# Kernel optimization log

Hardware: AMD Instinct MI355X
Metric: run time of the kernel (lower is better)

## Reference

```python
import jax, jax.numpy as jnp
import numpy as np

B, S, H, NH = 2, 2048, 1024, 16
HD = H // NH
ROTARY_DIM = 64
EPS = 1e-5
MINUS_INF = -10000.0


def _apply_rotary(q, k, rotary_dim):
    # q, k: [B, S, NH, HD]; GPT-NeoX style rotate_half on first rotary_dim dims
    pos = jnp.arange(S, dtype=jnp.float32)
    inv_freq = 1.0 / (10000.0 ** (jnp.arange(0, rotary_dim, 2, dtype=jnp.float32) / rotary_dim))
    freqs = pos[:, None] * inv_freq[None, :]                      # [S, rd/2]
    cos = jnp.concatenate([jnp.cos(freqs)] * 2, -1)[None, :, None, :]  # [1,S,1,rd]
    sin = jnp.concatenate([jnp.sin(freqs)] * 2, -1)[None, :, None, :]

    def rot(t):
        t_rot, t_pass = t[..., :rotary_dim], t[..., rotary_dim:]
        t1, t2 = jnp.split(t_rot, 2, axis=-1)
        rotated = jnp.concatenate([-t2, t1], axis=-1)
        return jnp.concatenate([t_rot * cos + rotated * sin, t_pass], axis=-1)

    return rot(q), rot(k)


def setup_inputs() -> dict:
    key = jax.random.key(0)
    ks = jax.random.split(key, 6)
    w_scale = 0.02
    return {
        "x": jax.random.normal(ks[0], (B, S, H), jnp.float32),
        "input_mask": jnp.ones((B, S), jnp.int32),
        "norm_w": jnp.ones((H,), jnp.float32),
        "norm_b": jnp.zeros((H,), jnp.float32),
        "attn_qkvw": jax.random.normal(ks[1], (H, 3 * H), jnp.float32) * w_scale,
        "attn_qkvb": jax.random.normal(ks[2], (3 * H,), jnp.float32) * w_scale,
        "attn_ow": jax.random.normal(ks[3], (H, H), jnp.float32) * w_scale,
        "attn_ob": jax.random.normal(ks[4], (H,), jnp.float32) * w_scale,
    }


def reference(x, input_mask, norm_w, norm_b, attn_qkvw, attn_qkvb, attn_ow, attn_ob):
    # pre-layernorm (qkv_gemm path with config.pre_layer_norm)
    mu = x.mean(-1, keepdims=True)
    var = x.var(-1, keepdims=True)
    xn = (x - mu) * jax.lax.rsqrt(var + EPS) * norm_w + norm_b

    # fused QKV projection
    qkv = xn @ attn_qkvw + attn_qkvb                       # [B,S,3H]
    q, k, v = jnp.split(qkv, 3, axis=-1)
    q = q.reshape(B, S, NH, HD)
    k = k.reshape(B, S, NH, HD)
    v = v.reshape(B, S, NH, HD)

    # rotary embedding on q,k
    q, k = _apply_rotary(q, k, ROTARY_DIM)

    # scaled scores + mask bias (1 - mask) * -10000 + triangular masking
    scale = 1.0 / np.sqrt(HD).astype(np.float32)
    scores = jnp.einsum("bqhd,bkhd->bhqk", q, k) * scale   # [B,NH,S,S]
    mask_bias = (1.0 - input_mask.astype(scores.dtype)) * MINUS_INF
    scores = scores + mask_bias[:, None, None, :]
    causal = jnp.tril(jnp.ones((S, S), bool))
    scores = jnp.where(causal[None, None], scores, MINUS_INF)

    probs = jax.nn.softmax(scores, axis=-1)
    ctx = jnp.einsum("bhqk,bkhd->bqhd", probs, v).reshape(B, S, H)

    # output projection (vector_matmul + bias)
    return ctx @ attn_ow + attn_ob
```

## Files before the change

kernel.cpp:

```cpp
#include <hip/hip_runtime.h>
#include <hip/hip_bf16.h>

#define B_  2
#define S_  2048
#define H_  1024
#define NH_ 16
#define HD_ 64
#define T_  (B_*S_)
#define H3_ (3*H_)

typedef float  floatx4 __attribute__((ext_vector_type(4)));
typedef __bf16 bf16x8  __attribute__((ext_vector_type(8)));

__device__ inline unsigned short f2bf_rn(float f) {
    union { float f; unsigned int u; } v; v.f = f;
    unsigned int u = v.u;
    u += 0x7fffu + ((u >> 16) & 1u);
    return (unsigned short)(u >> 16);
}
__device__ inline unsigned short f2bf_tr(float f) {
    union { float f; unsigned int u; } v; v.f = f;
    return (unsigned short)(v.u >> 16);
}
__device__ inline floatx4 fzero4() { floatx4 v; v[0]=0.f; v[1]=0.f; v[2]=0.f; v[3]=0.f; return v; }

__device__ inline void gload_lds16(const unsigned short* g, unsigned short* l) {
    __builtin_amdgcn_global_load_lds((const __attribute__((address_space(1))) unsigned int*)g,
                                     (__attribute__((address_space(3))) unsigned int*)l,
                                     16, 0, 0);
}

#define TLD 72
__global__ __launch_bounds__(256) void cvt_both_k(const float* __restrict__ qkvw,
                                                  const float* __restrict__ ow,
                                                  unsigned short* __restrict__ qkvwT,
                                                  unsigned short* __restrict__ owT) {
    __shared__ unsigned short Ts[64 * TLD];
    int id = blockIdx.x;
    const float* W; unsigned short* Wt; int N, nb, kb;
    if (id < 768) { W = qkvw; Wt = qkvwT; N = H3_; nb = (id % 48) * 64; kb = (id / 48) * 64; }
    else { id -= 768; W = ow; Wt = owT; N = H_; nb = (id % 16) * 64; kb = (id / 16) * 64; }
    const int K = H_;
    const int tid = threadIdx.x;
    #pragma unroll
    for (int p = 0; p < 4; p++) {
        const int krow = kb + p * 16 + (tid >> 4);
        const int ncol = (tid & 15) * 4;
        const float4 w = *reinterpret_cast<const float4*>(&W[(size_t)krow * N + nb + ncol]);
        Ts[(ncol + 0) * TLD + p * 16 + (tid >> 4)] = f2bf_rn(w.x);
        Ts[(ncol + 1) * TLD + p * 16 + (tid >> 4)] = f2bf_rn(w.y);
        Ts[(ncol + 2) * TLD + p * 16 + (tid >> 4)] = f2bf_rn(w.z);
        Ts[(ncol + 3) * TLD + p * 16 + (tid >> 4)] = f2bf_rn(w.w);
    }
    __syncthreads();
    #pragma unroll
    for (int p = 0; p < 2; p++) {
        const int n = (tid >> 3) + p * 32;
        const int k8 = (tid & 7) * 8;
        const uint4 v = *reinterpret_cast<const uint4*>(&Ts[n * TLD + k8]);
        *reinterpret_cast<uint4*>(&Wt[(size_t)(nb + n) * K + kb + k8]) = v;
    }
}

__global__ __launch_bounds__(256) void layernorm_k(const float* __restrict__ x,
                                                   const float* __restrict__ w,
                                                   const float* __restrict__ b,
                                                   unsigned short* __restrict__ xn) {
    const int t   = blockIdx.x;
    const int tid = threadIdx.x;
    const float4 v = reinterpret_cast<const float4*>(x + (size_t)t * H_)[tid];
    float s  = v.x + v.y + v.z + v.w;
    float s2 = v.x*v.x + v.y*v.y + v.z*v.z + v.w*v.w;
    for (int off = 32; off > 0; off >>= 1) {
        s  += __shfl_down(s,  off, 64);
        s2 += __shfl_down(s2, off, 64);
    }
    __shared__ float red[8];
    const int wave = tid >> 6, lane = tid & 63;
    if (lane == 0) { red[wave] = s; red[4 + wave] = s2; }
    __syncthreads();
    if (tid == 0) {
        red[0] = red[0] + red[1] + red[2] + red[3];
        red[4] = red[4] + red[5] + red[6] + red[7];
    }
    __syncthreads();
    const float mean = red[0] * (1.f / H_);
    const float var  = red[4] * (1.f / H_) - mean * mean;
    const float rstd = rsqrtf(var + 1e-5f);
    const float4 wv = reinterpret_cast<const float4*>(w)[tid];
    const float4 bv = reinterpret_cast<const float4*>(b)[tid];
    ushort4 o = make_ushort4(f2bf_rn((v.x - mean) * rstd * wv.x + bv.x),
                             f2bf_rn((v.y - mean) * rstd * wv.y + bv.y),
                             f2bf_rn((v.z - mean) * rstd * wv.z + bv.z),
                             f2bf_rn((v.w - mean) * rstd * wv.w + bv.w));
    reinterpret_cast<ushort4*>(xn + (size_t)t * H_)[tid] = o;
}

#define BM 128
#define BN 128

__device__ inline void gemm_core(const unsigned short* __restrict__ A,
                                 const unsigned short* __restrict__ Bt,
                                 int K, int mBase, int nBase,
                                 int tid, floatx4 acc[4][4],
                                 unsigned short* As0, unsigned short* As1,
                                 unsigned short* Bs0, unsigned short* Bs1) {
    const int lane = tid & 63;
    const int wave = tid >> 6;
    const int wr = wave >> 1, wc = wave & 1;
    const int srow = lane >> 2;
    const int scol = (lane & 3) * 8;
    const int mrow = lane & 15;
    const int koff = (lane >> 4) * 8;

    for (int kb = 0; kb < K; kb += 64) {
        __syncthreads();
        #pragma unroll
        for (int p = 0; p < 2; p++) {
            const int r = wave * 16 + p * 64;
            const size_t ga = (size_t)(mBase + r + srow) * K + kb + scol;
            const size_t gb = (size_t)(nBase + r + srow) * K + kb + scol;
            gload_lds16(&A [ga],      &As0[r * 32]);
            gload_lds16(&A [ga + 32], &As1[r * 32]);
            gload_lds16(&Bt[gb],      &Bs0[r * 32]);
            gload_lds16(&Bt[gb + 32], &Bs1[r * 32]);
        }
        __syncthreads();

        #pragma unroll
        for (int half = 0; half < 2; half++) {
            const unsigned short* As = half ? As1 : As0;
            const unsigned short* Bs = half ? Bs1 : Bs0;
            bf16x8 afrag[4], bfrag[4];
            #pragma unroll
            for (int mt = 0; mt < 4; mt++)
                afrag[mt] = *reinterpret_cast<const bf16x8*>(&As[(wr * 64 + mt * 16 + mrow) * 32 + koff]);
            #pragma unroll
            for (int nt = 0; nt < 4; nt++)
                bfrag[nt] = *reinterpret_cast<const bf16x8*>(&Bs[(wc * 64 + nt * 16 + mrow) * 32 + koff]);
            #pragma unroll
            for (int mt = 0; mt < 4; mt++)
                #pragma unroll
                for (int nt = 0; nt < 4; nt++)
                    acc[mt][nt] = __builtin_amdgcn_mfma_f32_16x16x32_bf16(afrag[mt], bfrag[nt], acc[mt][nt], 0, 0, 0);
        }
    }
}

__global__ __launch_bounds__(256) void gemm_qkv_k(const unsigned short* __restrict__ A,
                                                  const unsigned short* __restrict__ Bt,
                                                  const float* __restrict__ bias,
                                                  unsigned short* __restrict__ Qo,
                                                  unsigned short* __restrict__ Ko,
                                                  unsigned short* __restrict__ Vto) {
    __shared__ unsigned short As0[BM * 32], As1[BM * 32];
    __shared__ unsigned short Bs0[BN * 32], Bs1[BN * 32];

    const int tid  = threadIdx.x;
    const int lane = tid & 63;
    const int wave = tid >> 6;
    const int wr = wave >> 1, wc = wave & 1;
    const int mBase = blockIdx.y * BM;
    const int nBase = blockIdx.x * BN;

    floatx4 acc[4][4];
    #pragma unroll
    for (int i = 0; i < 4; i++)
        #pragma unroll
        for (int j = 0; j < 4; j++) acc[i][j] = fzero4();

    gemm_core(A, Bt, H_, mBase, nBase, tid, acc, As0, As1, Bs0, Bs1);

    const int col0 = lane & 15;
    const int r0   = (lane >> 4) * 4;
    const int hg   = (nBase + wc * 64) >> 6;
    const int sec  = hg >> 4;
    const int h    = hg & 15;

    float bs[4];
    #pragma unroll
    for (int nt = 0; nt < 4; nt++) bs[nt] = bias[nBase + wc * 64 + nt * 16 + col0];

    if (sec < 2) {
        unsigned short* dst = (sec == 0) ? Qo : Ko;
        const float if0 = __expf((float)col0        * (-0.2878231366f));
        const float if1 = __expf((float)(16 + col0) * (-0.2878231366f));
        #pragma unroll
        for (int mt = 0; mt < 4; mt++) {
            #pragma unroll
            for (int reg = 0; reg < 4; reg++) {
                const int t  = mBase + wr * 64 + mt * 16 + r0 + reg;
                const int bb = t >> 11;
                const int s  = t & (S_ - 1);
                float sn0, cs0, sn1, cs1;
                __sincosf((float)s * if0, &sn0, &cs0);
                __sincosf((float)s * if1, &sn1, &cs1);
                const float v0 = acc[mt][0][reg] + bs[0];
                const float v1 = acc[mt][1][reg] + bs[1];
                const float v2 = acc[mt][2][reg] + bs[2];
                const float v3 = acc[mt][3][reg] + bs[3];
                const float o0 = v0 * cs0 - v2 * sn0;
                const float o1 = v1 * cs1 - v3 * sn1;
                const float o2 = v2 * cs0 + v0 * sn0;
                const float o3 = v3 * cs1 + v1 * sn1;
                const size_t rb = ((size_t)(bb * NH_ + h) * S_ + s) * HD_;
                dst[rb +      col0] = f2bf_rn(o0);
                dst[rb + 16 + col0] = f2bf_rn(o1);
                dst[rb + 32 + col0] = f2bf_rn(o2);
                dst[rb + 48 + col0] = f2bf_rn(o3);
            }
        }
    } else {
        #pragma unroll
        for (int mt = 0; mt < 4; mt++) {
            const int t0 = mBase + wr * 64 + mt * 16 + r0;
            const int bb = t0 >> 11;
            const int s0 = t0 & (S_ - 1);
            #pragma unroll
            for (int nt = 0; nt < 4; nt++) {
                const int d = nt * 16 + col0;
                ushort4 o;
                o.x = f2bf_rn(acc[mt][nt][0] + bs[nt]);
                o.y = f2bf_rn(acc[mt][nt][1] + bs[nt]);
                o.z = f2bf_rn(acc[mt][nt][2] + bs[nt]);
                o.w = f2bf_rn(acc[mt][nt][3] + bs[nt]);
                *reinterpret_cast<ushort4*>(&Vto[((size_t)(bb * NH_ + h) * HD_ + d) * S_ + s0]) = o;
            }
        }
    }
}

__global__ __launch_bounds__(256) void gemm_proj_k(const unsigned short* __restrict__ A,
                                                   const unsigned short* __restrict__ Bt,
                                                   const float* __restrict__ bias,
                                                   float* __restrict__ Cf,
                                                   int M, int N, int K) {
    __shared__ unsigned short As0[BM * 32], As1[BM * 32];
    __shared__ unsigned short Bs0[BN * 32], Bs1[BN * 32];

    const int tid  = threadIdx.x;
    const int lane = tid & 63;
    const int wave = tid >> 6;
    const int wr = wave >> 1, wc = wave & 1;
    const int mBase = blockIdx.y * BM;
    const int nBase = blockIdx.x * BN;

    floatx4 acc[4][4];
    #pragma unroll
    for (int i = 0; i < 4; i++)
        #pragma unroll
        for (int j = 0; j < 4; j++) acc[i][j] = fzero4();

    gemm_core(A, Bt, K, mBase, nBase, tid, acc, As0, As1, Bs0, Bs1);

    const int col0 = lane & 15;
    const int r0   = (lane >> 4) * 4;
    #pragma unroll
    for (int mt = 0; mt < 4; mt++) {
        #pragma unroll
        for (int nt = 0; nt < 4; nt++) {
            const int gcol = nBase + wc * 64 + nt * 16 + col0;
            const float bsv = bias[gcol];
            #pragma unroll
            for (int reg = 0; reg < 4; reg++) {
                const int grow = mBase + wr * 64 + mt * 16 + r0 + reg;
                Cf[(size_t)grow * N + gcol] = acc[mt][nt][reg] + bsv;
            }
        }
    }
}

#define ALD 72
#define SCL2 0.1803368801f
#define MNEG -14427.0f

__global__ __launch_bounds__(256, 3) void attn_k(const unsigned short* __restrict__ Q,
                                                 const unsigned short* __restrict__ Kg,
                                                 const unsigned short* __restrict__ Vt,
                                                 const int* __restrict__ mask,
                                                 unsigned short* __restrict__ ctx) {
    const int id = blockIdx.x;
    const int bh = id & 31;
    const int v  = 31 - (id >> 5);
    const int b  = bh >> 4;
    const int h  = bh & 15;
    const int tid  = threadIdx.x;
    const int lane = tid & 63;
    const int wave = tid >> 6;

    __shared__ unsigned short Ks [2][64 * ALD];
    __shared__ unsigned short Vts[2][64 * ALD];
    __shared__ unsigned short Ps[4][16 * ALD];

    const size_t base = (size_t)bh * S_ * HD_;
    const int qbase = v * 64 + wave * 16;
    const int mrow = lane & 15;
    const int koff = (lane >> 4) * 8;
    const int r0   = (lane >> 4) * 4;
    const int col0 = lane & 15;

    bf16x8 qf0 = *reinterpret_cast<const bf16x8*>(&Q[base + (size_t)(qbase + mrow) * HD_ + koff]);
    bf16x8 qf1 = *reinterpret_cast<const bf16x8*>(&Q[base + (size_t)(qbase + mrow) * HD_ + 32 + koff]);

    bf16x8 onesf;
    {
        const __bf16 ov = (__bf16)((mrow == 0) ? 1.f : 0.f);
        #pragma unroll
        for (int q = 0; q < 8; q++) onesf[q] = ov;
    }

    floatx4 Oacc[4];
    floatx4 Lacc = fzero4();
    #pragma unroll
    for (int nt = 0; nt < 4; nt++) Oacc[nt] = fzero4();

    const int srow = tid >> 3;
    const int scol = (tid & 7) * 8;

    uint4 k00, k01, k10, k11, v00, v01, v10, v11;
    float mb00, mb01, mb02, mb03, mb10, mb11, mb12, mb13;
#define PF_TILE(TT, KR0, KR1, VR0, VR1, M0, M1, M2, M3) do {                                   \
        const int kb_ = (TT) * 64;                                                             \
        KR0 = *reinterpret_cast<const uint4*>(&Kg[base + (size_t)(kb_ + srow)      * HD_ + scol]); \
        KR1 = *reinterpret_cast<const uint4*>(&Kg[base + (size_t)(kb_ + srow + 32) * HD_ + scol]); \
        VR0 = *reinterpret_cast<const uint4*>(&Vt[base + (size_t)srow        * S_ + kb_ + scol]);  \
        VR1 = *reinterpret_cast<const uint4*>(&Vt[base + (size_t)(srow + 32) * S_ + kb_ + scol]);  \
        M0 = (1.f - (float)mask[b * S_ + kb_ +  0 + col0]) * MNEG;                             \
        M1 = (1.f - (float)mask[b * S_ + kb_ + 16 + col0]) * MNEG;                             \
        M2 = (1.f - (float)mask[b * S_ + kb_ + 32 + col0]) * MNEG;                             \
        M3 = (1.f - (float)mask[b * S_ + kb_ + 48 + col0]) * MNEG;                             \
    } while (0)
#define PREFETCH_MACRO(MI) do {                                                                \
        const int t0_ = min(2 * (MI), v);                                                      \
        const int t1_ = min(2 * (MI) + 1, v);                                                  \
        PF_TILE(t0_, k00, k01, v00, v01, mb00, mb01, mb02, mb03);                              \
        PF_TILE(t1_, k10, k11, v10, v11, mb10, mb11, mb12, mb13);                              \
    } while (0)

    const int nmac = (v + 2) >> 1;
    PREFETCH_MACRO(0);

    unsigned short* pw = Ps[wave];

    for (int mi = 0; mi < nmac; mi++) {
        if (mi) __syncthreads();
        *reinterpret_cast<uint4*>(&Ks [0][ srow       * ALD + scol]) = k00;
        *reinterpret_cast<uint4*>(&Ks [0][(srow + 32) * ALD + scol]) = k01;
        *reinterpret_cast<uint4*>(&Ks [1][ srow       * ALD + scol]) = k10;
        *reinterpret_cast<uint4*>(&Ks [1][(srow + 32) * ALD + scol]) = k11;
        *reinterpret_cast<uint4*>(&Vts[0][ srow       * ALD + scol]) = v00;
        *reinterpret_cast<uint4*>(&Vts[0][(srow + 32) * ALD + scol]) = v01;
        *reinterpret_cast<uint4*>(&Vts[1][ srow       * ALD + scol]) = v10;
        *reinterpret_cast<uint4*>(&Vts[1][(srow + 32) * ALD + scol]) = v11;
        __syncthreads();
        const float mc00 = mb00, mc01 = mb01, mc02 = mb02, mc03 = mb03;
        const float mc10 = mb10, mc11 = mb11, mc12 = mb12, mc13 = mb13;
        if (mi + 1 < nmac) PREFETCH_MACRO(mi + 1);

        #pragma unroll
        for (int half = 0; half < 2; half++) {
            const int kt = 2 * mi + half;
            if (half && kt > v) continue;
            const int kb = kt * 64;
            const unsigned short* ks = Ks [half];
            const unsigned short* vs = Vts[half];
            const float c0 = half ? mc10 : mc00;
            const float c1 = half ? mc11 : mc01;
            const float c2 = half ? mc12 : mc02;
            const float c3 = half ? mc13 : mc03;

            floatx4 sc[4];
            #pragma unroll
            for (int nt = 0; nt < 4; nt++) {
                const bf16x8 kf0 = *reinterpret_cast<const bf16x8*>(&ks[(nt * 16 + mrow) * ALD + koff]);
                const bf16x8 kf1 = *reinterpret_cast<const bf16x8*>(&ks[(nt * 16 + mrow) * ALD + 32 + koff]);
                floatx4 c = fzero4();
                c = __builtin_amdgcn_mfma_f32_16x16x32_bf16(qf0, kf0, c, 0, 0, 0);
                c = __builtin_amdgcn_mfma_f32_16x16x32_bf16(qf1, kf1, c, 0, 0, 0);
                sc[nt] = c;
            }
            #pragma unroll
            for (int nt = 0; nt < 4; nt++) {
                const float mbv = (nt == 0) ? c0 : (nt == 1) ? c1 : (nt == 2) ? c2 : c3;
                #pragma unroll
                for (int reg = 0; reg < 4; reg++)
                    sc[nt][reg] = sc[nt][reg] * SCL2 + mbv;
            }
            if (kt == v) {
                #pragma unroll
                for (int nt = 0; nt < 4; nt++) {
                    const int key = kb + nt * 16 + col0;
                    #pragma unroll
                    for (int reg = 0; reg < 4; reg++)
                        if (key > qbase + r0 + reg) sc[nt][reg] = MNEG;
                }
            }
            #pragma unroll
            for (int nt = 0; nt < 4; nt++)
                #pragma unroll
                for (int reg = 0; reg < 4; reg++)
                    pw[(r0 + reg) * ALD + nt * 16 + col0] = f2bf_tr(exp2f(sc[nt][reg]));
            const bf16x8 p0 = *reinterpret_cast<const bf16x8*>(&pw[mrow * ALD + koff]);
            const bf16x8 p1 = *reinterpret_cast<const bf16x8*>(&pw[mrow * ALD + 32 + koff]);
            #pragma unroll
            for (int nt = 0; nt < 4; nt++) {
                const bf16x8 vf0 = *reinterpret_cast<const bf16x8*>(&vs[(nt * 16 + mrow) * ALD + koff]);
                const bf16x8 vf1 = *reinterpret_cast<const bf16x8*>(&vs[(nt * 16 + mrow) * ALD + 32 + koff]);
                Oacc[nt] = __builtin_amdgcn_mfma_f32_16x16x32_bf16(p0, vf0, Oacc[nt], 0, 0, 0);
                Oacc[nt] = __builtin_amdgcn_mfma_f32_16x16x32_bf16(p1, vf1, Oacc[nt], 0, 0, 0);
            }
            Lacc = __builtin_amdgcn_mfma_f32_16x16x32_bf16(p0, onesf, Lacc, 0, 0, 0);
            Lacc = __builtin_amdgcn_mfma_f32_16x16x32_bf16(p1, onesf, Lacc, 0, 0, 0);
        }
    }
#undef PREFETCH_MACRO
#undef PF_TILE

    float rl[4];
    #pragma unroll
    for (int reg = 0; reg < 4; reg++) {
        const float lsum = __shfl(Lacc[reg], lane & 48, 64);
        rl[reg] = 1.f / lsum;
    }
    #pragma unroll
    for (int nt = 0; nt < 4; nt++)
        #pragma unroll
        for (int reg = 0; reg < 4; reg++) {
            const int q = qbase + r0 + reg;
            const int d = nt * 16 + col0;
            ctx[((size_t)b * S_ + q) * H_ + h * HD_ + d] = f2bf_rn(Oacc[nt][reg] * rl[reg]);
        }
}

extern "C" void kernel_launch(void* const* d_in, const int* in_sizes, int n_in,
                              void* d_out, int out_size, void* d_ws, size_t ws_size,
                              hipStream_t stream) {
    const float* x     = (const float*)d_in[0];
    const int*   mask  = (const int*)d_in[1];
    const float* normw = (const float*)d_in[2];
    const float* normb = (const float*)d_in[3];
    const float* qkvw  = (const float*)d_in[4];
    const float* qkvb  = (const float*)d_in[5];
    const float* ow    = (const float*)d_in[6];
    const float* ob    = (const float*)d_in[7];
    float* out = (float*)d_out;

    char* ws = (char*)d_ws;
    unsigned short* xn_bf   = (unsigned short*)(ws);
    unsigned short* qkvwT   = (unsigned short*)(ws + (8ull  << 20));
    unsigned short* owT     = (unsigned short*)(ws + (14ull << 20));
    unsigned short* Qb      = (unsigned short*)(ws + (16ull << 20));
    unsigned short* Kb      = (unsigned short*)(ws + (24ull << 20));
    unsigned short* Vtb     = (unsigned short*)(ws + (32ull << 20));
    unsigned short* ctx_bf  = (unsigned short*)(ws + (40ull << 20));

    cvt_both_k<<<1024, 256, 0, stream>>>(qkvw, ow, qkvwT, owT);
    layernorm_k<<<T_, 256, 0, stream>>>(x, normw, normb, xn_bf);
    gemm_qkv_k<<<dim3(H3_ / BN, T_ / BM), 256, 0, stream>>>(xn_bf, qkvwT, qkvb, Qb, Kb, Vtb);
    attn_k<<<1024, 256, 0, stream>>>(Qb, Kb, Vtb, mask, ctx_bf);
    gemm_proj_k<<<dim3(H_ / BN, T_ / BM), 256, 0, stream>>>(ctx_bf, owT, ob, out, T_, H_, H_);
}
```

Before: 200.6 us.

## Double attention query tile per block to 128 rows and reorder causal blocks

Each wave now processes 32 query rows (two 16-row MFMA groups) instead of 16, so a block covers 128 queries. Each K/V tile loaded into shared memory is therefore reused for twice as many score and PV MFMAs, cutting global loads and LDS staging per query. The grid is halved to 512 blocks, and the block order is remapped so the first 256 blocks go from heavy to light work and the rest from light to heavy, to balance the causal workload. In exchange it doubles accumulator registers and lowers the occupancy hint from 3 to 2 blocks, and the coarser tiles raise the tail imbalance.

```diff
diff --git a/kernel.cpp b/kernel.cpp
--- a/kernel.cpp
+++ b/kernel.cpp
@@ -274,14 +274,15 @@
 #define SCL2 0.1803368801f
 #define MNEG -14427.0f
 
-__global__ __launch_bounds__(256, 3) void attn_k(const unsigned short* __restrict__ Q,
+__global__ __launch_bounds__(256, 2) void attn_k(const unsigned short* __restrict__ Q,
                                                  const unsigned short* __restrict__ Kg,
                                                  const unsigned short* __restrict__ Vt,
                                                  const int* __restrict__ mask,
                                                  unsigned short* __restrict__ ctx) {
     const int id = blockIdx.x;
-    const int bh = id & 31;
-    const int v  = 31 - (id >> 5);
+    int bh, v;
+    if (id < 256) { bh = id & 31; v = 15 - (id >> 5); }
+    else { const int i2 = id - 256; bh = i2 & 31; v = i2 >> 5; }
     const int b  = bh >> 4;
     const int h  = bh & 15;
     const int tid  = threadIdx.x;
@@ -290,17 +291,21 @@
 
     __shared__ unsigned short Ks [2][64 * ALD];
     __shared__ unsigned short Vts[2][64 * ALD];
-    __shared__ unsigned short Ps[4][16 * ALD];
+    __shared__ unsigned short Ps [4][32 * ALD];
 
     const size_t base = (size_t)bh * S_ * HD_;
-    const int qbase = v * 64 + wave * 16;
+    const int qbase = v * 128 + wave * 32;
     const int mrow = lane & 15;
     const int koff = (lane >> 4) * 8;
     const int r0   = (lane >> 4) * 4;
     const int col0 = lane & 15;
 
-    bf16x8 qf0 = *reinterpret_cast<const bf16x8*>(&Q[base + (size_t)(qbase + mrow) * HD_ + koff]);
-    bf16x8 qf1 = *reinterpret_cast<const bf16x8*>(&Q[base + (size_t)(qbase + mrow) * HD_ + 32 + koff]);
+    bf16x8 qf[2][2];
+    #pragma unroll
+    for (int mg = 0; mg < 2; mg++) {
+        qf[mg][0] = *reinterpret_cast<const bf16x8*>(&Q[base + (size_t)(qbase + mg * 16 + mrow) * HD_ + koff]);
+        qf[mg][1] = *reinterpret_cast<const bf16x8*>(&Q[base + (size_t)(qbase + mg * 16 + mrow) * HD_ + 32 + koff]);
+    }
 
     bf16x8 onesf;
     {
@@ -309,13 +314,20 @@
         for (int q = 0; q < 8; q++) onesf[q] = ov;
     }
 
-    floatx4 Oacc[4];
-    floatx4 Lacc = fzero4();
-    #pragma unroll
-    for (int nt = 0; nt < 4; nt++) Oacc[nt] = fzero4();
+    floatx4 Oacc[2][4];
+    floatx4 Lacc[2];
+    #pragma unroll
+    for (int mg = 0; mg < 2; mg++) {
+        Lacc[mg] = fzero4();
+        #pragma unroll
+        for (int nt = 0; nt < 4; nt++) Oacc[mg][nt] = fzero4();
+    }
 
     const int srow = tid >> 3;
     const int scol = (tid & 7) * 8;
+
+    const int vmaxt = 2 * v + 1;
+    const int vlast = 2 * v + (wave >> 1);
 
     uint4 k00, k01, k10, k11, v00, v01, v10, v11;
     float mb00, mb01, mb02, mb03, mb10, mb11, mb12, mb13;
@@ -331,13 +343,13 @@
         M3 = (1.f - (float)mask[b * S_ + kb_ + 48 + col0]) * MNEG;                             \
     } while (0)
 #define PREFETCH_MACRO(MI) do {                                                                \
-        const int t0_ = min(2 * (MI), v);                                                      \
-        const int t1_ = min(2 * (MI) + 1, v);                                                  \
+        const int t0_ = min(2 * (MI), vmaxt);                                                  \
+        const int t1_ = min(2 * (MI) + 1, vmaxt);                                              \
         PF_TILE(t0_, k00, k01, v00, v01, mb00, mb01, mb02, mb03);                              \
         PF_TILE(t1_, k10, k11, v10, v11, mb10, mb11, mb12, mb13);                              \
     } while (0)
 
-    const int nmac = (v + 2) >> 1;
+    const int nmac = v + 1;
     PREFETCH_MACRO(0);
 
     unsigned short* pw = Ps[wave];
@@ -360,7 +372,7 @@
         #pragma unroll
         for (int half = 0; half < 2; half++) {
             const int kt = 2 * mi + half;
-            if (half && kt > v) continue;
+            if (half && kt > vlast) continue;
             const int kb = kt * 64;
             const unsigned short* ks = Ks [half];
             const unsigned short* vs = Vts[half];
@@ -369,67 +381,89 @@
             const float c2 = half ? mc12 : mc02;
             const float c3 = half ? mc13 : mc03;
 
-            floatx4 sc[4];
+            floatx4 sc[2][4];
             #pragma unroll
             for (int nt = 0; nt < 4; nt++) {
                 const bf16x8 kf0 = *reinterpret_cast<const bf16x8*>(&ks[(nt * 16 + mrow) * ALD + koff]);
                 const bf16x8 kf1 = *reinterpret_cast<const bf16x8*>(&ks[(nt * 16 + mrow) * ALD + 32 + koff]);
-                floatx4 c = fzero4();
-                c = __builtin_amdgcn_mfma_f32_16x16x32_bf16(qf0, kf0, c, 0, 0, 0);
-                c = __builtin_amdgcn_mfma_f32_16x16x32_bf16(qf1, kf1, c, 0, 0, 0);
-                sc[nt] = c;
-            }
-            #pragma unroll
-            for (int nt = 0; nt < 4; nt++) {
-                const float mbv = (nt == 0) ? c0 : (nt == 1) ? c1 : (nt == 2) ? c2 : c3;
-                #pragma unroll
-                for (int reg = 0; reg < 4; reg++)
-                    sc[nt][reg] = sc[nt][reg] * SCL2 + mbv;
-            }
-            if (kt == v) {
+                #pragma unroll
+                for (int mg = 0; mg < 2; mg++) {
+                    floatx4 c = fzero4();
+                    c = __builtin_amdgcn_mfma_f32_16x16x32_bf16(qf[mg][0], kf0, c, 0, 0, 0);
+                    c = __builtin_amdgcn_mfma_f32_16x16x32_bf16(qf[mg][1], kf1, c, 0, 0, 0);
+                    sc[mg][nt] = c;
+                }
+            }
+            #pragma unroll
+            for (int mg = 0; mg < 2; mg++)
                 #pragma unroll
                 for (int nt = 0; nt < 4; nt++) {
-                    const int key = kb + nt * 16 + col0;
+                    const float mbv = (nt == 0) ? c0 : (nt == 1) ? c1 : (nt == 2) ? c2 : c3;
                     #pragma unroll
                     for (int reg = 0; reg < 4; reg++)
-                        if (key > qbase + r0 + reg) sc[nt][reg] = MNEG;
+                        sc[mg][nt][reg] = sc[mg][nt][reg] * SCL2 + mbv;
                 }
-            }
-            #pragma unroll
-            for (int nt = 0; nt < 4; nt++)
-                #pragma unroll
-                for (int reg = 0; reg < 4; reg++)
-                    pw[(r0 + reg) * ALD + nt * 16 + col0] = f2bf_tr(exp2f(sc[nt][reg]));
-            const bf16x8 p0 = *reinterpret_cast<const bf16x8*>(&pw[mrow * ALD + koff]);
-            const bf16x8 p1 = *reinterpret_cast<const bf16x8*>(&pw[mrow * ALD + 32 + koff]);
+            if (kt == vlast) {
+                #pragma unroll
+                for (int mg = 0; mg < 2; mg++)
+                    #pragma unroll
+                    for (int nt = 0; nt < 4; nt++) {
+                        const int key = kb + nt * 16 + col0;
+                        #pragma unroll
+                        for (int reg = 0; reg < 4; reg++)
+                            if (key > qbase + mg * 16 + r0 + reg) sc[mg][nt][reg] = MNEG;
+                    }
+            }
+            #pragma unroll
+            for (int mg = 0; mg < 2; mg++)
+                #pragma unroll
+                for (int nt = 0; nt < 4; nt++)
+                    #pragma unroll
+                    for (int reg = 0; reg < 4; reg++)
+                        pw[(mg * 16 + r0 + reg) * ALD + nt * 16 + col0] = f2bf_tr(exp2f(sc[mg][nt][reg]));
+            bf16x8 p0[2], p1[2];
+            #pragma unroll
+            for (int mg = 0; mg < 2; mg++) {
+                p0[mg] = *reinterpret_cast<const bf16x8*>(&pw[(mg * 16 + mrow) * ALD + koff]);
+                p1[mg] = *reinterpret_cast<const bf16x8*>(&pw[(mg * 16 + mrow) * ALD + 32 + koff]);
+            }
             #pragma unroll
             for (int nt = 0; nt < 4; nt++) {
                 const bf16x8 vf0 = *reinterpret_cast<const bf16x8*>(&vs[(nt * 16 + mrow) * ALD + koff]);
                 const bf16x8 vf1 = *reinterpret_cast<const bf16x8*>(&vs[(nt * 16 + mrow) * ALD + 32 + koff]);
-                Oacc[nt] = __builtin_amdgcn_mfma_f32_16x16x32_bf16(p0, vf0, Oacc[nt], 0, 0, 0);
-                Oacc[nt] = __builtin_amdgcn_mfma_f32_16x16x32_bf16(p1, vf1, Oacc[nt], 0, 0, 0);
-            }
-            Lacc = __builtin_amdgcn_mfma_f32_16x16x32_bf16(p0, onesf, Lacc, 0, 0, 0);
-            Lacc = __builtin_amdgcn_mfma_f32_16x16x32_bf16(p1, onesf, Lacc, 0, 0, 0);
+                #pragma unroll
+                for (int mg = 0; mg < 2; mg++) {
+                    Oacc[mg][nt] = __builtin_amdgcn_mfma_f32_16x16x32_bf16(p0[mg], vf0, Oacc[mg][nt], 0, 0, 0);
+                    Oacc[mg][nt] = __builtin_amdgcn_mfma_f32_16x16x32_bf16(p1[mg], vf1, Oacc[mg][nt], 0, 0, 0);
+                }
+            }
+            #pragma unroll
+            for (int mg = 0; mg < 2; mg++) {
+                Lacc[mg] = __builtin_amdgcn_mfma_f32_16x16x32_bf16(p0[mg], onesf, Lacc[mg], 0, 0, 0);
+                Lacc[mg] = __builtin_amdgcn_mfma_f32_16x16x32_bf16(p1[mg], onesf, Lacc[mg], 0, 0, 0);
+            }
         }
     }
 #undef PREFETCH_MACRO
 #undef PF_TILE
 
-    float rl[4];
-    #pragma unroll
-    for (int reg = 0; reg < 4; reg++) {
-        const float lsum = __shfl(Lacc[reg], lane & 48, 64);
-        rl[reg] = 1.f / lsum;
-    }
-    #pragma unroll
-    for (int nt = 0; nt < 4; nt++)
+    #pragma unroll
+    for (int mg = 0; mg < 2; mg++) {
+        float rl[4];
         #pragma unroll
         for (int reg = 0; reg < 4; reg++) {
-            const int q = qbase + r0 + reg;
-            const int d = nt * 16 + col0;
-            ctx[((size_t)b * S_ + q) * H_ + h * HD_ + d] = f2bf_rn(Oacc[nt][reg] * rl[reg]);
-        }
+            const float lsum = __shfl(Lacc[mg][reg], lane & 48, 64);
+            rl[reg] = 1.f / lsum;
+        }
+        #pragma unroll
+        for (int nt = 0; nt < 4; nt++)
+            #pragma unroll
+            for (int reg = 0; reg < 4; reg++) {
+                const int q = qbase + mg * 16 + r0 + reg;
+                const int d = nt * 16 + col0;
+                ctx[((size_t)b * S_ + q) * H_ + h * HD_ + d] = f2bf_rn(Oacc[mg][nt][reg] * rl[reg]);
+            }
+    }
 }
 
 extern "C" void kernel_launch(void* const* d_in, const int* in_sizes, int n_in,
@@ -457,6 +491,6 @@
     cvt_both_k<<<1024, 256, 0, stream>>>(qkvw, ow, qkvwT, owT);
     layernorm_k<<<T_, 256, 0, stream>>>(x, normw, normb, xn_bf);
     gemm_qkv_k<<<dim3(H3_ / BN, T_ / BM), 256, 0, stream>>>(xn_bf, qkvwT, qkvb, Qb, Kb, Vtb);
-    attn_k<<<1024, 256, 0, stream>>>(Qb, Kb, Vtb, mask, ctx_bf);
+    attn_k<<<512, 256, 0, stream>>>(Qb, Kb, Vtb, mask, ctx_bf);
     gemm_proj_k<<<dim3(H_ / BN, T_ / BM), 256, 0, stream>>>(ctx_bf, owT, ob, out, T_, H_, H_);
 }
```

Measured after the change: 208.6 us. 1.04x slower.

## Load K and V fragments directly from global memory in attention kernel

Applied to the files above, without the earlier changes.

Removes the shared-memory staging of K and V tiles, the register prefetch pipeline and the block-wide barriers. Each wave now reads its MFMA operand fragments for K and Vt straight from global memory, relying on L1/L2 to serve the reuse across the four waves. Occupancy is also raised from 3 to 4 blocks per CU. In exchange it loses explicit prefetch overlap and issues four times the global/L1 traffic for K and V, since the waves no longer share a staged copy.

```diff
diff --git a/kernel.cpp b/kernel.cpp
--- a/kernel.cpp
+++ b/kernel.cpp
@@ -274,7 +274,7 @@
 #define SCL2 0.1803368801f
 #define MNEG -14427.0f
 
-__global__ __launch_bounds__(256, 3) void attn_k(const unsigned short* __restrict__ Q,
+__global__ __launch_bounds__(256, 4) void attn_k(const unsigned short* __restrict__ Q,
                                                  const unsigned short* __restrict__ Kg,
                                                  const unsigned short* __restrict__ Vt,
                                                  const int* __restrict__ mask,
@@ -288,8 +288,6 @@
     const int lane = tid & 63;
     const int wave = tid >> 6;
 
-    __shared__ unsigned short Ks [2][64 * ALD];
-    __shared__ unsigned short Vts[2][64 * ALD];
     __shared__ unsigned short Ps[4][16 * ALD];
 
     const size_t base = (size_t)bh * S_ * HD_;
@@ -299,8 +297,8 @@
     const int r0   = (lane >> 4) * 4;
     const int col0 = lane & 15;
 
-    bf16x8 qf0 = *reinterpret_cast<const bf16x8*>(&Q[base + (size_t)(qbase + mrow) * HD_ + koff]);
-    bf16x8 qf1 = *reinterpret_cast<const bf16x8*>(&Q[base + (size_t)(qbase + mrow) * HD_ + 32 + koff]);
+    const bf16x8 qf0 = *reinterpret_cast<const bf16x8*>(&Q[base + (size_t)(qbase + mrow) * HD_ + koff]);
+    const bf16x8 qf1 = *reinterpret_cast<const bf16x8*>(&Q[base + (size_t)(qbase + mrow) * HD_ + 32 + koff]);
 
     bf16x8 onesf;
     {
@@ -314,107 +312,59 @@
     #pragma unroll
     for (int nt = 0; nt < 4; nt++) Oacc[nt] = fzero4();
 
-    const int srow = tid >> 3;
-    const int scol = (tid & 7) * 8;
-
-    uint4 k00, k01, k10, k11, v00, v01, v10, v11;
-    float mb00, mb01, mb02, mb03, mb10, mb11, mb12, mb13;
-#define PF_TILE(TT, KR0, KR1, VR0, VR1, M0, M1, M2, M3) do {                                   \
-        const int kb_ = (TT) * 64;                                                             \
-        KR0 = *reinterpret_cast<const uint4*>(&Kg[base + (size_t)(kb_ + srow)      * HD_ + scol]); \
-        KR1 = *reinterpret_cast<const uint4*>(&Kg[base + (size_t)(kb_ + srow + 32) * HD_ + scol]); \
-        VR0 = *reinterpret_cast<const uint4*>(&Vt[base + (size_t)srow        * S_ + kb_ + scol]);  \
-        VR1 = *reinterpret_cast<const uint4*>(&Vt[base + (size_t)(srow + 32) * S_ + kb_ + scol]);  \
-        M0 = (1.f - (float)mask[b * S_ + kb_ +  0 + col0]) * MNEG;                             \
-        M1 = (1.f - (float)mask[b * S_ + kb_ + 16 + col0]) * MNEG;                             \
-        M2 = (1.f - (float)mask[b * S_ + kb_ + 32 + col0]) * MNEG;                             \
-        M3 = (1.f - (float)mask[b * S_ + kb_ + 48 + col0]) * MNEG;                             \
-    } while (0)
-#define PREFETCH_MACRO(MI) do {                                                                \
-        const int t0_ = min(2 * (MI), v);                                                      \
-        const int t1_ = min(2 * (MI) + 1, v);                                                  \
-        PF_TILE(t0_, k00, k01, v00, v01, mb00, mb01, mb02, mb03);                              \
-        PF_TILE(t1_, k10, k11, v10, v11, mb10, mb11, mb12, mb13);                              \
-    } while (0)
-
-    const int nmac = (v + 2) >> 1;
-    PREFETCH_MACRO(0);
-
     unsigned short* pw = Ps[wave];
 
-    for (int mi = 0; mi < nmac; mi++) {
-        if (mi) __syncthreads();
-        *reinterpret_cast<uint4*>(&Ks [0][ srow       * ALD + scol]) = k00;
-        *reinterpret_cast<uint4*>(&Ks [0][(srow + 32) * ALD + scol]) = k01;
-        *reinterpret_cast<uint4*>(&Ks [1][ srow       * ALD + scol]) = k10;
-        *reinterpret_cast<uint4*>(&Ks [1][(srow + 32) * ALD + scol]) = k11;
-        *reinterpret_cast<uint4*>(&Vts[0][ srow       * ALD + scol]) = v00;
-        *reinterpret_cast<uint4*>(&Vts[0][(srow + 32) * ALD + scol]) = v01;
-        *reinterpret_cast<uint4*>(&Vts[1][ srow       * ALD + scol]) = v10;
-        *reinterpret_cast<uint4*>(&Vts[1][(srow + 32) * ALD + scol]) = v11;
-        __syncthreads();
-        const float mc00 = mb00, mc01 = mb01, mc02 = mb02, mc03 = mb03;
-        const float mc10 = mb10, mc11 = mb11, mc12 = mb12, mc13 = mb13;
-        if (mi + 1 < nmac) PREFETCH_MACRO(mi + 1);
-
-        #pragma unroll
-        for (int half = 0; half < 2; half++) {
-            const int kt = 2 * mi + half;
-            if (half && kt > v) continue;
-            const int kb = kt * 64;
-            const unsigned short* ks = Ks [half];
-            const unsigned short* vs = Vts[half];
-            const float c0 = half ? mc10 : mc00;
-            const float c1 = half ? mc11 : mc01;
-            const float c2 = half ? mc12 : mc02;
-            const float c3 = half ? mc13 : mc03;
-
-            floatx4 sc[4];
+    for (int kt = 0; kt <= v; kt++) {
+        const int kb = kt * 64;
+
+        const float c0 = (1.f - (float)mask[b * S_ + kb +  0 + col0]) * MNEG;
+        const float c1 = (1.f - (float)mask[b * S_ + kb + 16 + col0]) * MNEG;
+        const float c2 = (1.f - (float)mask[b * S_ + kb + 32 + col0]) * MNEG;
+        const float c3 = (1.f - (float)mask[b * S_ + kb + 48 + col0]) * MNEG;
+
+        floatx4 sc[4];
+        #pragma unroll
+        for (int nt = 0; nt < 4; nt++) {
+            const bf16x8 kf0 = *reinterpret_cast<const bf16x8*>(&Kg[base + (size_t)(kb + nt * 16 + mrow) * HD_ + koff]);
+            const bf16x8 kf1 = *reinterpret_cast<const bf16x8*>(&Kg[base + (size_t)(kb + nt * 16 + mrow) * HD_ + 32 + koff]);
+            floatx4 c = fzero4();
+            c = __builtin_amdgcn_mfma_f32_16x16x32_bf16(qf0, kf0, c, 0, 0, 0);
+            c = __builtin_amdgcn_mfma_f32_16x16x32_bf16(qf1, kf1, c, 0, 0, 0);
+            sc[nt] = c;
+        }
+        #pragma unroll
+        for (int nt = 0; nt < 4; nt++) {
+            const float mbv = (nt == 0) ? c0 : (nt == 1) ? c1 : (nt == 2) ? c2 : c3;
+            #pragma unroll
+            for (int reg = 0; reg < 4; reg++)
+                sc[nt][reg] = sc[nt][reg] * SCL2 + mbv;
+        }
+        if (kt == v) {
             #pragma unroll
             for (int nt = 0; nt < 4; nt++) {
-                const bf16x8 kf0 = *reinterpret_cast<const bf16x8*>(&ks[(nt * 16 + mrow) * ALD + koff]);
-                const bf16x8 kf1 = *reinterpret_cast<const bf16x8*>(&ks[(nt * 16 + mrow) * ALD + 32 + koff]);
-                floatx4 c = fzero4();
-                c = __builtin_amdgcn_mfma_f32_16x16x32_bf16(qf0, kf0, c, 0, 0, 0);
-                c = __builtin_amdgcn_mfma_f32_16x16x32_bf16(qf1, kf1, c, 0, 0, 0);
-                sc[nt] = c;
-            }
-            #pragma unroll
-            for (int nt = 0; nt < 4; nt++) {
-                const float mbv = (nt == 0) ? c0 : (nt == 1) ? c1 : (nt == 2) ? c2 : c3;
+                const int key = kb + nt * 16 + col0;
                 #pragma unroll
                 for (int reg = 0; reg < 4; reg++)
-                    sc[nt][reg] = sc[nt][reg] * SCL2 + mbv;
+                    if (key > qbase + r0 + reg) sc[nt][reg] = MNEG;
             }
-            if (kt == v) {
-                #pragma unroll
-                for (int nt = 0; nt < 4; nt++) {
-                    const int key = kb + nt * 16 + col0;
-                    #pragma unroll
-                    for (int reg = 0; reg < 4; reg++)
-                        if (key > qbase + r0 + reg) sc[nt][reg] = MNEG;
-                }
-            }
-            #pragma unroll
-            for (int nt = 0; nt < 4; nt++)
-                #pragma unroll
-                for (int reg = 0; reg < 4; reg++)
-                    pw[(r0 + reg) * ALD + nt * 16 + col0] = f2bf_tr(exp2f(sc[nt][reg]));
-            const bf16x8 p0 = *reinterpret_cast<const bf16x8*>(&pw[mrow * ALD + koff]);
-            const bf16x8 p1 = *reinterpret_cast<const bf16x8*>(&pw[mrow * ALD + 32 + koff]);
-            #pragma unroll
-            for (int nt = 0; nt < 4; nt++) {
-                const bf16x8 vf0 = *reinterpret_cast<const bf16x8*>(&vs[(nt * 16 + mrow) * ALD + koff]);
-                const bf16x8 vf1 = *reinterpret_cast<const bf16x8*>(&vs[(nt * 16 + mrow) * ALD + 32 + koff]);
-                Oacc[nt] = __builtin_amdgcn_mfma_f32_16x16x32_bf16(p0, vf0, Oacc[nt], 0, 0, 0);
-                Oacc[nt] = __builtin_amdgcn_mfma_f32_16x16x32_bf16(p1, vf1, Oacc[nt], 0, 0, 0);
-            }
-            Lacc = __builtin_amdgcn_mfma_f32_16x16x32_bf16(p0, onesf, Lacc, 0, 0, 0);
-            Lacc = __builtin_amdgcn_mfma_f32_16x16x32_bf16(p1, onesf, Lacc, 0, 0, 0);
-        }
-    }
-#undef PREFETCH_MACRO
-#undef PF_TILE
+        }
+        #pragma unroll
+        for (int nt = 0; nt < 4; nt++)
+            #pragma unroll
+            for (int reg = 0; reg < 4; reg++)
+                pw[(r0 + reg) * ALD + nt * 16 + col0] = f2bf_tr(exp2f(sc[nt][reg]));
+        const bf16x8 p0 = *reinterpret_cast<const bf16x8*>(&pw[mrow * ALD + koff]);
+        const bf16x8 p1 = *reinterpret_cast<const bf16x8*>(&pw[mrow * ALD + 32 + koff]);
+        #pragma unroll
+        for (int nt = 0; nt < 4; nt++) {
+            const bf16x8 vf0 = *reinterpret_cast<const bf16x8*>(&Vt[base + (size_t)(nt * 16 + mrow) * S_ + kb + koff]);
+            const bf16x8 vf1 = *reinterpret_cast<const bf16x8*>(&Vt[base + (size_t)(nt * 16 + mrow) * S_ + kb + 32 + koff]);
+            Oacc[nt] = __builtin_amdgcn_mfma_f32_16x16x32_bf16(p0, vf0, Oacc[nt], 0, 0, 0);
+            Oacc[nt] = __builtin_amdgcn_mfma_f32_16x16x32_bf16(p1, vf1, Oacc[nt], 0, 0, 0);
+        }
+        Lacc = __builtin_amdgcn_mfma_f32_16x16x32_bf16(p0, onesf, Lacc, 0, 0, 0);
+        Lacc = __builtin_amdgcn_mfma_f32_16x16x32_bf16(p1, onesf, Lacc, 0, 0, 0);
+    }
 
     float rl[4];
     #pragma unroll
```

Result: slower. 308.4 us (+53.7%).

## Use 512-thread attention blocks covering 128 queries with shared K/V tiles

Applied to the files above, without the earlier changes.

The attention kernel now runs 8 waves per block, each handling 16 query rows, so a block covers 128 queries instead of 64. Each K/V tile loaded into LDS is reused by twice as many waves, and each thread now stages one row per tile instead of two, which halves global traffic per query. Block ordering is changed to interleave heavy and light causal blocks across the two halves of the grid. The cost is larger blocks, doubled P scratch in LDS, and causal imbalance within a block: the first four waves skip the final tile while the other waves process it.

```diff
diff --git a/kernel.cpp b/kernel.cpp
--- a/kernel.cpp
+++ b/kernel.cpp
@@ -274,14 +274,15 @@
 #define SCL2 0.1803368801f
 #define MNEG -14427.0f
 
-__global__ __launch_bounds__(256, 3) void attn_k(const unsigned short* __restrict__ Q,
+__global__ __launch_bounds__(512, 4) void attn_k(const unsigned short* __restrict__ Q,
                                                  const unsigned short* __restrict__ Kg,
                                                  const unsigned short* __restrict__ Vt,
                                                  const int* __restrict__ mask,
                                                  unsigned short* __restrict__ ctx) {
     const int id = blockIdx.x;
-    const int bh = id & 31;
-    const int v  = 31 - (id >> 5);
+    int bh, v;
+    if (id < 256) { bh = id & 31; v = 15 - (id >> 5); }
+    else { const int i2 = id - 256; bh = i2 & 31; v = i2 >> 5; }
     const int b  = bh >> 4;
     const int h  = bh & 15;
     const int tid  = threadIdx.x;
@@ -290,17 +291,17 @@
 
     __shared__ unsigned short Ks [2][64 * ALD];
     __shared__ unsigned short Vts[2][64 * ALD];
-    __shared__ unsigned short Ps[4][16 * ALD];
+    __shared__ unsigned short Ps [8][16 * ALD];
 
     const size_t base = (size_t)bh * S_ * HD_;
-    const int qbase = v * 64 + wave * 16;
+    const int qbase = v * 128 + wave * 16;
     const int mrow = lane & 15;
     const int koff = (lane >> 4) * 8;
     const int r0   = (lane >> 4) * 4;
     const int col0 = lane & 15;
 
-    bf16x8 qf0 = *reinterpret_cast<const bf16x8*>(&Q[base + (size_t)(qbase + mrow) * HD_ + koff]);
-    bf16x8 qf1 = *reinterpret_cast<const bf16x8*>(&Q[base + (size_t)(qbase + mrow) * HD_ + 32 + koff]);
+    const bf16x8 qf0 = *reinterpret_cast<const bf16x8*>(&Q[base + (size_t)(qbase + mrow) * HD_ + koff]);
+    const bf16x8 qf1 = *reinterpret_cast<const bf16x8*>(&Q[base + (size_t)(qbase + mrow) * HD_ + 32 + koff]);
 
     bf16x8 onesf;
     {
@@ -317,41 +318,38 @@
     const int srow = tid >> 3;
     const int scol = (tid & 7) * 8;
 
-    uint4 k00, k01, k10, k11, v00, v01, v10, v11;
+    const int vmaxt = 2 * v + 1;
+    const int vlast = 2 * v + (wave >> 2);
+
+    uint4 k0, v0, k1, v1;
     float mb00, mb01, mb02, mb03, mb10, mb11, mb12, mb13;
-#define PF_TILE(TT, KR0, KR1, VR0, VR1, M0, M1, M2, M3) do {                                   \
+#define PF_TILE(TT, KR, VR, M0, M1, M2, M3) do {                                               \
         const int kb_ = (TT) * 64;                                                             \
-        KR0 = *reinterpret_cast<const uint4*>(&Kg[base + (size_t)(kb_ + srow)      * HD_ + scol]); \
-        KR1 = *reinterpret_cast<const uint4*>(&Kg[base + (size_t)(kb_ + srow + 32) * HD_ + scol]); \
-        VR0 = *reinterpret_cast<const uint4*>(&Vt[base + (size_t)srow        * S_ + kb_ + scol]);  \
-        VR1 = *reinterpret_cast<const uint4*>(&Vt[base + (size_t)(srow + 32) * S_ + kb_ + scol]);  \
+        KR = *reinterpret_cast<const uint4*>(&Kg[base + (size_t)(kb_ + srow) * HD_ + scol]);   \
+        VR = *reinterpret_cast<const uint4*>(&Vt[base + (size_t)srow * S_ + kb_ + scol]);      \
         M0 = (1.f - (float)mask[b * S_ + kb_ +  0 + col0]) * MNEG;                             \
         M1 = (1.f - (float)mask[b * S_ + kb_ + 16 + col0]) * MNEG;                             \
         M2 = (1.f - (float)mask[b * S_ + kb_ + 32 + col0]) * MNEG;                             \
         M3 = (1.f - (float)mask[b * S_ + kb_ + 48 + col0]) * MNEG;                             \
     } while (0)
 #define PREFETCH_MACRO(MI) do {                                                                \
-        const int t0_ = min(2 * (MI), v);                                                      \
-        const int t1_ = min(2 * (MI) + 1, v);                                                  \
-        PF_TILE(t0_, k00, k01, v00, v01, mb00, mb01, mb02, mb03);                              \
-        PF_TILE(t1_, k10, k11, v10, v11, mb10, mb11, mb12, mb13);                              \
+        const int t0_ = min(2 * (MI), vmaxt);                                                  \
+        const int t1_ = min(2 * (MI) + 1, vmaxt);                                              \
+        PF_TILE(t0_, k0, v0, mb00, mb01, mb02, mb03);                                          \
+        PF_TILE(t1_, k1, v1, mb10, mb11, mb12, mb13);                                          \
     } while (0)
 
-    const int nmac = (v + 2) >> 1;
+    const int nmac = v + 1;
     PREFETCH_MACRO(0);
 
     unsigned short* pw = Ps[wave];
 
     for (int mi = 0; mi < nmac; mi++) {
         if (mi) __syncthreads();
-        *reinterpret_cast<uint4*>(&Ks [0][ srow       * ALD + scol]) = k00;
-        *reinterpret_cast<uint4*>(&Ks [0][(srow + 32) * ALD + scol]) = k01;
-        *reinterpret_cast<uint4*>(&Ks [1][ srow       * ALD + scol]) = k10;
-        *reinterpret_cast<uint4*>(&Ks [1][(srow + 32) * ALD + scol]) = k11;
-        *reinterpret_cast<uint4*>(&Vts[0][ srow       * ALD + scol]) = v00;
-        *reinterpret_cast<uint4*>(&Vts[0][(srow + 32) * ALD + scol]) = v01;
-        *reinterpret_cast<uint4*>(&Vts[1][ srow       * ALD + scol]) = v10;
-        *reinterpret_cast<uint4*>(&Vts[1][(srow + 32) * ALD + scol]) = v11;
+        *reinterpret_cast<uint4*>(&Ks [0][srow * ALD + scol]) = k0;
+        *reinterpret_cast<uint4*>(&Ks [1][srow * ALD + scol]) = k1;
+        *reinterpret_cast<uint4*>(&Vts[0][srow * ALD + scol]) = v0;
+        *reinterpret_cast<uint4*>(&Vts[1][srow * ALD + scol]) = v1;
         __syncthreads();
         const float mc00 = mb00, mc01 = mb01, mc02 = mb02, mc03 = mb03;
         const float mc10 = mb10, mc11 = mb11, mc12 = mb12, mc13 = mb13;
@@ -360,7 +358,7 @@
         #pragma unroll
         for (int half = 0; half < 2; half++) {
             const int kt = 2 * mi + half;
-            if (half && kt > v) continue;
+            if (half && kt > vlast) continue;
             const int kb = kt * 64;
             const unsigned short* ks = Ks [half];
             const unsigned short* vs = Vts[half];
@@ -386,7 +384,7 @@
                 for (int reg = 0; reg < 4; reg++)
                     sc[nt][reg] = sc[nt][reg] * SCL2 + mbv;
             }
-            if (kt == v) {
+            if (kt == vlast) {
                 #pragma unroll
                 for (int nt = 0; nt < 4; nt++) {
                     const int key = kb + nt * 16 + col0;
@@ -457,6 +455,6 @@
     cvt_both_k<<<1024, 256, 0, stream>>>(qkvw, ow, qkvwT, owT);
     layernorm_k<<<T_, 256, 0, stream>>>(x, normw, normb, xn_bf);
     gemm_qkv_k<<<dim3(H3_ / BN, T_ / BM), 256, 0, stream>>>(xn_bf, qkvwT, qkvb, Qb, Kb, Vtb);
-    attn_k<<<1024, 256, 0, stream>>>(Qb, Kb, Vtb, mask, ctx_bf);
+    attn_k<<<512, 512, 0, stream>>>(Qb, Kb, Vtb, mask, ctx_bf);
     gemm_proj_k<<<dim3(H_ / BN, T_ / BM), 256, 0, stream>>>(ctx_bf, owT, ob, out, T_, H_, H_);
 }
```

New measurement: 201.5 us. No clear change (+0.4%).
